# Kernel optimization log

Hardware: AMD Instinct MI355X
Metric: run time of the kernel (lower is better)

The kernel has to match this reference:

```python
import jax, jax.numpy as jnp
import numpy as np

D_MODEL = 1024
NUM_HEADS = 16
HEAD_DIM = D_MODEL // NUM_HEADS


def setup_inputs() -> dict:
    key = jax.random.key(0)
    k_x, k_wqkv, k_bqkv, k_wo, k_bo = jax.random.split(key, 5)
    x = jax.random.normal(k_x, (2, 2048, D_MODEL), dtype=jnp.float32)
    s = 1.0 / np.sqrt(D_MODEL)
    W_qkv = jax.random.uniform(k_wqkv, (D_MODEL, 3 * D_MODEL), jnp.float32, -s, s)
    b_qkv = jax.random.uniform(k_bqkv, (3 * D_MODEL,), jnp.float32, -s, s)
    W_o = jax.random.uniform(k_wo, (D_MODEL, D_MODEL), jnp.float32, -s, s)
    b_o = jax.random.uniform(k_bo, (D_MODEL,), jnp.float32, -s, s)
    return {"x": x, "W_qkv": W_qkv, "b_qkv": b_qkv, "W_o": W_o, "b_o": b_o}


def reference(x, W_qkv, b_qkv, W_o, b_o):
    B, S, D = x.shape
    # fused QKV projection: [B,S,3D]
    qkv = jnp.einsum('bsd,de->bse', x, W_qkv) + b_qkv
    # [B,S,H,3*hd] -> [B,H,S,3*hd]
    qkv = qkv.reshape(B, S, NUM_HEADS, 3 * HEAD_DIM).transpose(0, 2, 1, 3)
    q, k, v = jnp.split(qkv, 3, axis=-1)  # each [B,H,S,hd]
    scale = 1.0 / jnp.sqrt(jnp.asarray(HEAD_DIM, dtype=x.dtype))
    scores = jnp.einsum('bhqd,bhkd->bhqk', q, k) * scale  # [B,H,S,S]
    attn = jax.nn.softmax(scores, axis=-1)
    values = jnp.einsum('bhqk,bhkd->bhqd', attn, v)  # [B,H,S,hd]
    values = values.transpose(0, 2, 1, 3).reshape(B, S, D)
    out = jnp.einsum('bsd,de->bse', values, W_o) + b_o
    return out
```

## Files before the change

kernel.cpp:

```cpp
#include <hip/hip_runtime.h>
#include <stdint.h>
#include <stddef.h>

typedef _Float16 f16;
typedef _Float16 f16x8 __attribute__((ext_vector_type(8)));
typedef _Float16 f16x4 __attribute__((ext_vector_type(4)));
typedef float    f32x2 __attribute__((ext_vector_type(2)));
typedef float    f32x4 __attribute__((ext_vector_type(4)));
typedef float    f32x16 __attribute__((ext_vector_type(16)));
typedef int      i32x4 __attribute__((ext_vector_type(4)));
typedef int      i32x2 __attribute__((ext_vector_type(2)));

#define S_LEN 2048
#define DM    1024
#define NH    16
#define HD    64
#define NTOK  4096
#define NQKV  3072
#define QSCALE 0.18033688011112042f

#if __has_builtin(__builtin_amdgcn_exp2f)
#define EXP2(x) __builtin_amdgcn_exp2f(x)
#else
#define EXP2(x) __expf((x) * 0.69314718055994531f)
#endif

__device__ __forceinline__ void gl_lds16(const void* g, void* l) {
  __builtin_amdgcn_global_load_lds(
      (const __attribute__((address_space(1))) void*)g,
      (__attribute__((address_space(3))) void*)l, 16, 0, 0);
}

__device__ __forceinline__ void pl32_swap(int& a, int& b) {
#if __has_builtin(__builtin_amdgcn_permlane32_swap)
  i32x2 r = __builtin_amdgcn_permlane32_swap(a, b, false, false);
  a = r.x; b = r.y;
#else
  asm volatile("v_permlane32_swap_b32 %0, %1" : "+v"(a), "+v"(b));
#endif
}

__device__ __forceinline__ float swap_half(float x, int hi) {
  int a = __builtin_bit_cast(int, x);
  int b = a;
  pl32_swap(a, b);
  return __builtin_bit_cast(float, hi ? a : b);
}

__device__ __forceinline__ int pkrtz(float a, float b) {
  auto h = __builtin_amdgcn_cvt_pkrtz(a, b);
  return __builtin_bit_cast(int, h);
}

__device__ __forceinline__ f16x8 mk_frag(int a, int b, int c, int d) {
  i32x4 v = {a, b, c, d};
  return __builtin_bit_cast(f16x8, v);
}

__device__ __forceinline__ f32x2 pk2(const f32x16& v, int i) {
  f32x2 r = {v[2*i], v[2*i+1]};
  return r;
}

__global__ __launch_bounds__(256) void cvt_f16_kernel(const float* __restrict__ in,
                                                      f16* __restrict__ out, int n) {
  int i = (blockIdx.x * 256 + threadIdx.x) * 8;
  if (i >= n) return;
  float4 a = *(const float4*)(in + i);
  float4 b = *(const float4*)(in + i + 4);
  f16x8 v = {(f16)a.x,(f16)a.y,(f16)a.z,(f16)a.w,(f16)b.x,(f16)b.y,(f16)b.z,(f16)b.w};
  *(f16x8*)(out + i) = v;
}

__global__ __launch_bounds__(256) void cvt_tr_kernel(const float* __restrict__ in,
                                                     f16* __restrict__ out, int R, int C) {
  __shared__ float t[32][33];
  int c0 = blockIdx.x * 32, r0 = blockIdx.y * 32;
  int tx = threadIdx.x, ty = threadIdx.y;
  #pragma unroll
  for (int i = 0; i < 4; ++i)
    t[ty + i*8][tx] = in[(size_t)(r0 + ty + i*8) * C + c0 + tx];
  __syncthreads();
  #pragma unroll
  for (int i = 0; i < 4; ++i)
    out[(size_t)(c0 + ty + i*8) * R + r0 + tx] = (f16)t[tx][ty + i*8];
}

template<int EPI>
__global__ __launch_bounds__(256) void gemm128_kernel(
    const f16* __restrict__ A, const f16* __restrict__ Bt,
    const float* __restrict__ bias,
    f16* __restrict__ qb, f16* __restrict__ kb, f16* __restrict__ vtb,
    float* __restrict__ out)
{
  __shared__ f16 As[128*32];
  __shared__ f16 Bs[128*32];
  const int tid = threadIdx.x;
  const int wid = tid >> 6, lane = tid & 63;
  const int g = lane >> 4, r = lane & 15;
  const int flat = blockIdx.x;
  const int xcd = flat & 7, idx = flat >> 3;
  const int m0 = (xcd * 4 + (idx & 3)) * 128;
  const int n0 = (idx >> 2) * 128;
  const int wm = (wid >> 1) * 64, wn = (wid & 1) * 64;

  f32x4 acc[4][4] = {};
  const int srow = tid >> 2;
  const int sch  = tid & 3;

  for (int kt = 0; kt < DM/32; ++kt) {
    const int k0 = kt * 32;
    __syncthreads();
    #pragma unroll
    for (int c = 0; c < 2; ++c) {
      int row = c*64 + srow;
      int sw = (sch ^ ((row >> 1) & 3)) * 8;
      gl_lds16(A  + (size_t)(m0 + row) * DM + k0 + sw, (char*)As + c*4096 + tid*16);
      gl_lds16(Bt + (size_t)(n0 + row) * DM + k0 + sw, (char*)Bs + c*4096 + tid*16);
    }
    __syncthreads();
    f16x8 a[4], b[4];
    #pragma unroll
    for (int mt = 0; mt < 4; ++mt) {
      int rl = wm + mt*16 + r;
      a[mt] = *(const f16x8*)(As + rl*32 + ((g ^ ((rl >> 1) & 3)) * 8));
    }
    #pragma unroll
    for (int nt = 0; nt < 4; ++nt) {
      int cl = wn + nt*16 + r;
      b[nt] = *(const f16x8*)(Bs + cl*32 + ((g ^ ((cl >> 1) & 3)) * 8));
    }
    #pragma unroll
    for (int mt = 0; mt < 4; ++mt)
      #pragma unroll
      for (int nt = 0; nt < 4; ++nt)
        acc[mt][nt] = __builtin_amdgcn_mfma_f32_16x16x32_f16(a[mt], b[nt], acc[mt][nt], 0, 0, 0);
  }

  if (EPI == 0) {
    #pragma unroll
    for (int mt = 0; mt < 4; ++mt) {
      int row0 = m0 + wm + mt*16 + g*4;
      int b_ = row0 >> 11, s0 = row0 & 2047;
      #pragma unroll
      for (int nt = 0; nt < 4; ++nt) {
        int col = n0 + wn + nt*16 + r;
        float bv = bias[col];
        int h = col / 192;
        int cc = col - h*192;
        int which = cc >> 6, d = cc & 63;
        size_t bh = (size_t)(b_*NH + h);
        if (which == 2) {
          f16x4 v;
          #pragma unroll
          for (int i = 0; i < 4; ++i) v[i] = (f16)(acc[mt][nt][i] + bv);
          *(f16x4*)(vtb + (bh*HD + d)*S_LEN + s0) = v;
        } else if (which == 0) {
          #pragma unroll
          for (int i = 0; i < 4; ++i)
            qb[(bh*S_LEN + s0 + i)*HD + d] = (f16)((acc[mt][nt][i] + bv) * QSCALE);
        } else {
          #pragma unroll
          for (int i = 0; i < 4; ++i)
            kb[(bh*S_LEN + s0 + i)*HD + d] = (f16)(acc[mt][nt][i] + bv);
        }
      }
    }
  } else {
    #pragma unroll
    for (int mt = 0; mt < 4; ++mt) {
      int row0 = m0 + wm + mt*16 + g*4;
      #pragma unroll
      for (int nt = 0; nt < 4; ++nt) {
        int col = n0 + wn + nt*16 + r;
        float bv = bias[col];
        #pragma unroll
        for (int i = 0; i < 4; ++i)
          out[(size_t)(row0 + i)*DM + col] = acc[mt][nt][i] + bv;
      }
    }
  }
}

__global__ __launch_bounds__(512, 4) void attn_kernel(
    const f16* __restrict__ qb, const f16* __restrict__ kb,
    const f16* __restrict__ vtb, f16* __restrict__ values)
{
  __shared__ __align__(16) char smem[66048];

  const int tid = threadIdx.x;
  const int wid = tid >> 6, lane = tid & 63;
  const int wq = wid & 3, wk = wid >> 2;
  const int ql = lane & 31, hi = lane >> 5;
  const int flat = blockIdx.x;
  const int xcd = flat & 7, idx = flat >> 3;
  const int bh = xcd * 4 + (idx & 3);
  const int q0 = (idx >> 2) * 128 + wq * 32;
  const f16* qh = qb  + (size_t)bh * S_LEN * HD;
  const f16* kh = kb  + (size_t)bh * S_LEN * HD;
  const f16* vh = vtb + (size_t)bh * HD * S_LEN;
  const int kbase0 = wk * 1024;
  const int htid = tid & 255;

  int koff[2], voff[2];
  #pragma unroll
  for (int c = 0; c < 2; ++c) {
    int ca = htid + c*256, pr = ca >> 4, pc = ca & 15, lc = pc ^ (pr & 15);
    int row2 = pr*2 + (lc >> 3), e8 = (lc & 7) * 8;
    koff[c] = row2 * HD + e8;
    voff[c] = row2 * S_LEN + e8;
  }

  f16x8 qf[4];
  #pragma unroll
  for (int dk = 0; dk < 4; ++dk)
    qf[dk] = *(const f16x8*)(qh + (size_t)(q0 + ql)*HD + dk*16 + hi*8);

  const int r0b = (ql >> 1) << 8;
  const int xv  = (ql >> 1) & 15;
  const int hb  = ((ql & 1) << 3) | hi;

  f32x2 lacc = {0.f, 0.f};
  f32x16 o0 = {}, o1 = {};
  f32x16 s0, s1;

  #define STAGE_K(kt_, buf_) do {                                          \
    const f16* ks_ = kh + (size_t)(kbase0 + (kt_)*64) * HD;                \
    char* kd_ = smem + (wk*2 + (buf_))*8192;                               \
    gl_lds16(ks_ + koff[0], kd_ + htid*16);                                \
    gl_lds16(ks_ + koff[1], kd_ + 4096 + htid*16);                         \
  } while (0)
  #define STAGE_V(kt_, buf_) do {                                          \
    const f16* vs_ = vh + (kbase0 + (kt_)*64);                             \
    char* vd_ = smem + 32768 + (wk*2 + (buf_))*8192;                       \
    gl_lds16(vs_ + voff[0], vd_ + htid*16);                                \
    gl_lds16(vs_ + voff[1], vd_ + 4096 + htid*16);                         \
  } while (0)

  #define QK(buf_) do {                                                    \
    const char* KsC = smem + (wk*2 + (buf_))*8192;                         \
    s0 = (f32x16){}; s1 = (f32x16){};                                      \
    __builtin_amdgcn_s_setprio(1);                                         \
    _Pragma("unroll")                                                      \
    for (int dk = 0; dk < 4; ++dk) {                                       \
      int off = r0b + (((hb | (dk << 1)) ^ xv) << 4);                      \
      f16x8 kf0 = *(const f16x8*)(KsC + off);                              \
      f16x8 kf1 = *(const f16x8*)(KsC + 4096 + off);                       \
      s0 = __builtin_amdgcn_mfma_f32_32x32x16_f16(kf0, qf[dk], s0, 0, 0, 0);\
      s1 = __builtin_amdgcn_mfma_f32_32x32x16_f16(kf1, qf[dk], s1, 0, 0, 0);\
    }                                                                      \
    __builtin_amdgcn_s_setprio(0);                                         \
  } while (0)

  #define EXP_PACK() do {                                                  \
    _Pragma("unroll")                                                      \
    for (int i = 0; i < 16; ++i) s0[i] = EXP2(s0[i]);                      \
    _Pragma("unroll")                                                      \
    for (int i = 0; i < 16; ++i) s1[i] = EXP2(s1[i]);                      \
    f32x2 sm[8];                                                           \
    _Pragma("unroll")                                                      \
    for (int i = 0; i < 8; ++i) sm[i] = pk2(s0, i) + pk2(s1, i);           \
    _Pragma("unroll")                                                      \
    for (int i = 0; i < 4; ++i) sm[i] += sm[i+4];                          \
    sm[0] += sm[1]; sm[2] += sm[3]; sm[0] += sm[2];                        \
    lacc += sm[0];                                                         \
    {                                                                      \
      int a = pkrtz(s0[0], s0[1]), b = pkrtz(s0[2], s0[3]);                \
      int c = pkrtz(s0[4], s0[5]), d = pkrtz(s0[6], s0[7]);                \
      pl32_swap(a, c); pl32_swap(b, d);                                    \
      pf[0] = mk_frag(a, b, c, d);                                         \
      a = pkrtz(s0[8],  s0[9]);  b = pkrtz(s0[10], s0[11]);                \
      c = pkrtz(s0[12], s0[13]); d = pkrtz(s0[14], s0[15]);                \
      pl32_swap(a, c); pl32_swap(b, d);                                    \
      pf[1] = mk_frag(a, b, c, d);                                         \
      a = pkrtz(s1[0], s1[1]); b = pkrtz(s1[2], s1[3]);                    \
      c = pkrtz(s1[4], s1[5]); d = pkrtz(s1[6], s1[7]);                    \
      pl32_swap(a, c); pl32_swap(b, d);                                    \
      pf[2] = mk_frag(a, b, c, d);                                         \
      a = pkrtz(s1[8],  s1[9]);  b = pkrtz(s1[10], s1[11]);                \
      c = pkrtz(s1[12], s1[13]); d = pkrtz(s1[14], s1[15]);                \
      pl32_swap(a, c); pl32_swap(b, d);                                    \
      pf[3] = mk_frag(a, b, c, d);                                         \
    }                                                                      \
  } while (0)

  #define PV(buf_) do {                                                    \
    const char* VsC = smem + 32768 + (wk*2 + (buf_))*8192;                 \
    __builtin_amdgcn_s_setprio(1);                                         \
    _Pragma("unroll")                                                      \
    for (int w = 0; w < 4; ++w) {                                          \
      int off = r0b + (((hb | (w << 1)) ^ xv) << 4);                       \
      f16x8 vf0 = *(const f16x8*)(VsC + off);                              \
      f16x8 vf1 = *(const f16x8*)(VsC + 4096 + off);                       \
      o0 = __builtin_amdgcn_mfma_f32_32x32x16_f16(pf[w], vf0, o0, 0, 0, 0);\
      o1 = __builtin_amdgcn_mfma_f32_32x32x16_f16(pf[w], vf1, o1, 0, 0, 0);\
    }                                                                      \
    __builtin_amdgcn_s_setprio(0);                                         \
  } while (0)

  STAGE_K(0, 0); STAGE_V(0, 0); STAGE_K(1, 1);
  __syncthreads();
  f16x8 pf[4];
  QK(0);
  __syncthreads();

  for (int kt = 0; kt < 15; ++kt) {
    const int cur = kt & 1;
    STAGE_V(kt + 1, cur ^ 1);
    if (kt < 14) STAGE_K(kt + 2, cur);
    EXP_PACK();
    QK(cur ^ 1);
    PV(cur);
    __syncthreads();
  }
  EXP_PACK();
  PV(1);
  __syncthreads();

  #undef STAGE_K
  #undef STAGE_V
  #undef QK
  #undef EXP_PACK
  #undef PV

  float l_run = lacc.x + lacc.y;
  l_run += swap_half(l_run, hi);

  float* crow = ((float*)smem) + (wq*64 + lane)*36;
  float* cb   = (float*)(smem + 65536);
  if (wk == 1) {
    #pragma unroll
    for (int j = 0; j < 4; ++j) {
      f32x4 v0 = {o0[4*j], o0[4*j+1], o0[4*j+2], o0[4*j+3]};
      f32x4 v1 = {o1[4*j], o1[4*j+1], o1[4*j+2], o1[4*j+3]};
      *(f32x4*)(crow + j*4)      = v0;
      *(f32x4*)(crow + 16 + j*4) = v1;
    }
    crow[32] = l_run;
  }
  __syncthreads();
  if (wk == 0) {
    float inv = 1.0f / (l_run + crow[32]);
    cb[wq*32 + ql] = inv;
    f32x4 vinv[4], po0[4], po1[4];
    #pragma unroll
    for (int t = 0; t < 4; ++t) {
      vinv[t] = *(const f32x4*)&cb[wq*32 + hi*4 + t*8];
      po0[t]  = *(const f32x4*)(crow + t*4);
      po1[t]  = *(const f32x4*)(crow + 16 + t*4);
    }
    const int b_ = bh >> 4, h = bh & 15;
    #pragma unroll
    for (int t = 0; t < 4; ++t)
      #pragma unroll
      for (int i = 0; i < 4; ++i) {
        float v0 = (o0[t*4+i] + po0[t][i]) * vinv[t][i];
        float v1 = (o1[t*4+i] + po1[t][i]) * vinv[t][i];
        int qrow = q0 + 4*hi + 8*t + i;
        size_t base = (size_t)(b_*S_LEN + qrow) * DM + h*HD + ql;
        values[base]      = (f16)v0;
        values[base + 32] = (f16)v1;
      }
  }
}

extern "C" void kernel_launch(void* const* d_in, const int* in_sizes, int n_in,
                              void* d_out, int out_size, void* d_ws, size_t ws_size,
                              hipStream_t stream) {
  (void)in_sizes; (void)n_in; (void)out_size; (void)ws_size;
  const float* x    = (const float*)d_in[0];
  const float* Wqkv = (const float*)d_in[1];
  const float* bqkv = (const float*)d_in[2];
  const float* Wo   = (const float*)d_in[3];
  const float* bo   = (const float*)d_in[4];
  float* out = (float*)d_out;

  char* ws = (char*)d_ws;
  f16* x_h    = (f16*)(ws);
  f16* Wqkv_t = (f16*)(ws + ( 8ull<<20));
  f16* Wo_t   = (f16*)(ws + (14ull<<20));
  f16* qbuf   = (f16*)(ws + (16ull<<20));
  f16* kbuf   = (f16*)(ws + (24ull<<20));
  f16* vtbuf  = (f16*)(ws + (32ull<<20));
  f16* vals   = (f16*)(ws + (40ull<<20));

  cvt_f16_kernel<<<dim3(NTOK*DM/8/256), dim3(256), 0, stream>>>(x, x_h, NTOK*DM);
  cvt_tr_kernel<<<dim3(NQKV/32, DM/32), dim3(32, 8), 0, stream>>>(Wqkv, Wqkv_t, DM, NQKV);
  cvt_tr_kernel<<<dim3(DM/32, DM/32),  dim3(32, 8), 0, stream>>>(Wo, Wo_t, DM, DM);

  gemm128_kernel<0><<<dim3(768), dim3(256), 0, stream>>>(
      x_h, Wqkv_t, bqkv, qbuf, kbuf, vtbuf, nullptr);

  attn_kernel<<<dim3(512), dim3(512), 0, stream>>>(qbuf, kbuf, vtbuf, vals);

  gemm128_kernel<1><<<dim3(256), dim3(256), 0, stream>>>(
      vals, Wo_t, bo, nullptr, nullptr, nullptr, out);
}
```

Measured before the change: 118.6 us.

## Double-buffer score registers and interleave QK MFMA with softmax exp in attention loop

```diff
diff --git a/kernel.cpp b/kernel.cpp
--- a/kernel.cpp
+++ b/kernel.cpp
@@ -222,7 +222,7 @@
 
   f32x2 lacc = {0.f, 0.f};
   f32x16 o0 = {}, o1 = {};
-  f32x16 s0, s1;
+  f32x16 sX0, sX1, sY0, sY1;
 
   #define STAGE_K(kt_, buf_) do {                                          \
     const f16* ks_ = kh + (size_t)(kbase0 + (kt_)*64) * HD;                \
@@ -237,91 +237,86 @@
     gl_lds16(vs_ + voff[1], vd_ + 4096 + htid*16);                         \
   } while (0)
 
-  #define QK(buf_) do {                                                    \
-    const char* KsC = smem + (wk*2 + (buf_))*8192;                         \
-    s0 = (f32x16){}; s1 = (f32x16){};                                      \
-    __builtin_amdgcn_s_setprio(1);                                         \
+  #define QK_H(S_, KsC_, base_) do {                                       \
+    S_ = (f32x16){};                                                       \
     _Pragma("unroll")                                                      \
     for (int dk = 0; dk < 4; ++dk) {                                       \
       int off = r0b + (((hb | (dk << 1)) ^ xv) << 4);                      \
-      f16x8 kf0 = *(const f16x8*)(KsC + off);                              \
-      f16x8 kf1 = *(const f16x8*)(KsC + 4096 + off);                       \
-      s0 = __builtin_amdgcn_mfma_f32_32x32x16_f16(kf0, qf[dk], s0, 0, 0, 0);\
-      s1 = __builtin_amdgcn_mfma_f32_32x32x16_f16(kf1, qf[dk], s1, 0, 0, 0);\
+      f16x8 kf = *(const f16x8*)((KsC_) + (base_) + off);                  \
+      S_ = __builtin_amdgcn_mfma_f32_32x32x16_f16(kf, qf[dk], S_, 0, 0, 0);\
     }                                                                      \
-    __builtin_amdgcn_s_setprio(0);                                         \
-  } while (0)
-
-  #define EXP_PACK() do {                                                  \
+  } while (0)
+
+  #define EXP_H(S_, PFA_, PFB_) do {                                       \
     _Pragma("unroll")                                                      \
-    for (int i = 0; i < 16; ++i) s0[i] = EXP2(s0[i]);                      \
+    for (int i = 0; i < 16; ++i) S_[i] = EXP2(S_[i]);                      \
+    f32x2 sm[4];                                                           \
     _Pragma("unroll")                                                      \
-    for (int i = 0; i < 16; ++i) s1[i] = EXP2(s1[i]);                      \
-    f32x2 sm[8];                                                           \
-    _Pragma("unroll")                                                      \
-    for (int i = 0; i < 8; ++i) sm[i] = pk2(s0, i) + pk2(s1, i);           \
-    _Pragma("unroll")                                                      \
-    for (int i = 0; i < 4; ++i) sm[i] += sm[i+4];                          \
-    sm[0] += sm[1]; sm[2] += sm[3]; sm[0] += sm[2];                        \
-    lacc += sm[0];                                                         \
-    {                                                                      \
-      int a = pkrtz(s0[0], s0[1]), b = pkrtz(s0[2], s0[3]);                \
-      int c = pkrtz(s0[4], s0[5]), d = pkrtz(s0[6], s0[7]);                \
-      pl32_swap(a, c); pl32_swap(b, d);                                    \
-      pf[0] = mk_frag(a, b, c, d);                                         \
-      a = pkrtz(s0[8],  s0[9]);  b = pkrtz(s0[10], s0[11]);                \
-      c = pkrtz(s0[12], s0[13]); d = pkrtz(s0[14], s0[15]);                \
-      pl32_swap(a, c); pl32_swap(b, d);                                    \
-      pf[1] = mk_frag(a, b, c, d);                                         \
-      a = pkrtz(s1[0], s1[1]); b = pkrtz(s1[2], s1[3]);                    \
-      c = pkrtz(s1[4], s1[5]); d = pkrtz(s1[6], s1[7]);                    \
-      pl32_swap(a, c); pl32_swap(b, d);                                    \
-      pf[2] = mk_frag(a, b, c, d);                                         \
-      a = pkrtz(s1[8],  s1[9]);  b = pkrtz(s1[10], s1[11]);                \
-      c = pkrtz(s1[12], s1[13]); d = pkrtz(s1[14], s1[15]);                \
-      pl32_swap(a, c); pl32_swap(b, d);                                    \
-      pf[3] = mk_frag(a, b, c, d);                                         \
-    }                                                                      \
-  } while (0)
-
-  #define PV(buf_) do {                                                    \
-    const char* VsC = smem + 32768 + (wk*2 + (buf_))*8192;                 \
-    __builtin_amdgcn_s_setprio(1);                                         \
+    for (int i = 0; i < 4; ++i) sm[i] = pk2(S_, i) + pk2(S_, i + 4);       \
+    sm[0] += sm[1]; sm[2] += sm[3]; lacc += sm[0] + sm[2];                 \
+    int a = pkrtz(S_[0], S_[1]), b = pkrtz(S_[2], S_[3]);                  \
+    int c = pkrtz(S_[4], S_[5]), d = pkrtz(S_[6], S_[7]);                  \
+    pl32_swap(a, c); pl32_swap(b, d);                                      \
+    PFA_ = mk_frag(a, b, c, d);                                            \
+    a = pkrtz(S_[8],  S_[9]);  b = pkrtz(S_[10], S_[11]);                  \
+    c = pkrtz(S_[12], S_[13]); d = pkrtz(S_[14], S_[15]);                  \
+    pl32_swap(a, c); pl32_swap(b, d);                                      \
+    PFB_ = mk_frag(a, b, c, d);                                            \
+  } while (0)
+
+  #define PVQ(VsC_) do {                                                   \
     _Pragma("unroll")                                                      \
     for (int w = 0; w < 4; ++w) {                                          \
       int off = r0b + (((hb | (w << 1)) ^ xv) << 4);                       \
-      f16x8 vf0 = *(const f16x8*)(VsC + off);                              \
-      f16x8 vf1 = *(const f16x8*)(VsC + 4096 + off);                       \
+      f16x8 vf0 = *(const f16x8*)((VsC_) + off);                           \
+      f16x8 vf1 = *(const f16x8*)((VsC_) + 4096 + off);                    \
       o0 = __builtin_amdgcn_mfma_f32_32x32x16_f16(pf[w], vf0, o0, 0, 0, 0);\
       o1 = __builtin_amdgcn_mfma_f32_32x32x16_f16(pf[w], vf1, o1, 0, 0, 0);\
     }                                                                      \
-    __builtin_amdgcn_s_setprio(0);                                         \
+  } while (0)
+
+  #define BODY(SA0_, SA1_, SB0_, SB1_, kt_, cur_) do {                     \
+    const char* KsN = smem + (wk*2 + ((cur_) ^ 1))*8192;                   \
+    const char* VsC = smem + 32768 + (wk*2 + (cur_))*8192;                 \
+    STAGE_V((kt_) + 1, (cur_) ^ 1);                                        \
+    if ((kt_) < 14) STAGE_K((kt_) + 2, (cur_));                            \
+    QK_H(SB0_, KsN, 0);                                                    \
+    QK_H(SB1_, KsN, 4096);                                                 \
+    EXP_H(SA0_, pf[0], pf[1]);                                             \
+    EXP_H(SA1_, pf[2], pf[3]);                                             \
+    PVQ(VsC);                                                              \
+    __syncthreads();                                                       \
   } while (0)
 
   STAGE_K(0, 0); STAGE_V(0, 0); STAGE_K(1, 1);
   __syncthreads();
   f16x8 pf[4];
-  QK(0);
-  __syncthreads();
-
-  for (int kt = 0; kt < 15; ++kt) {
-    const int cur = kt & 1;
-    STAGE_V(kt + 1, cur ^ 1);
-    if (kt < 14) STAGE_K(kt + 2, cur);
-    EXP_PACK();
-    QK(cur ^ 1);
-    PV(cur);
-    __syncthreads();
-  }
-  EXP_PACK();
-  PV(1);
+  {
+    const char* Ks0 = smem + (wk*2)*8192;
+    QK_H(sX0, Ks0, 0);
+    QK_H(sX1, Ks0, 4096);
+  }
+  __syncthreads();
+
+  for (int kt2 = 0; kt2 < 14; kt2 += 2) {
+    BODY(sX0, sX1, sY0, sY1, kt2,     0);
+    BODY(sY0, sY1, sX0, sX1, kt2 + 1, 1);
+  }
+  BODY(sX0, sX1, sY0, sY1, 14, 0);
+  EXP_H(sY0, pf[0], pf[1]);
+  EXP_H(sY1, pf[2], pf[3]);
+  {
+    const char* VsC = smem + 32768 + (wk*2 + 1)*8192;
+    PVQ(VsC);
+  }
   __syncthreads();
 
   #undef STAGE_K
   #undef STAGE_V
-  #undef QK
-  #undef EXP_PACK
-  #undef PV
+  #undef QK_H
+  #undef EXP_H
+  #undef PVQ
+  #undef BODY
 
   float l_run = lacc.x + lacc.y;
   l_run += swap_half(l_run, hi);
```

Result: slower. 191.3 us (+61.3%).
